# Performance work log

Measured on AMD Instinct MI355X. Metric: run time of the kernel, lower is better.

## Reference

```python
import jax, jax.numpy as jnp
import numpy as np

HEADS = 8


def setup_inputs() -> dict:
    key = jax.random.key(0)
    k0, k1, k2, k3 = jax.random.split(key, 4)
    b, c, h, w = 8, 128, 32, 32
    x = jax.random.normal(k0, (b, c, h, w), dtype=jnp.float32)
    # torch nn.Linear weights: (out_features, in_features)
    s = c ** -0.5
    wq = jax.random.normal(k1, (c, c), dtype=jnp.float32) * s
    wk = jax.random.normal(k2, (c, c), dtype=jnp.float32) * s
    wv = jax.random.normal(k3, (c, c), dtype=jnp.float32) * s
    return {"x": x, "wq": wq, "wk": wk, "wv": wv}


def reference(x, wq, wk, wv):
    b, c, h, w = x.shape
    n = HEADS
    d = c // n
    scale = d ** -0.5
    xp = jnp.transpose(x, (0, 2, 3, 1))  # (b, h, w, c)
    # torch Linear: y = x @ W.T
    q = (xp @ wq.T).reshape(b, h, w, n, d)
    k = (xp @ wk.T).reshape(b, h, w, n, d)
    v = (xp @ wv.T).reshape(b, h, w, n, d)
    # full 2D spatial attention scores: (b, n, h, w, x, y)
    weights = jnp.einsum('bhwnd,bxynd->bnhwxy', q, k) * scale
    # NOTE: original softmaxes over the LAST spatial axis (y) only
    weights = jax.nn.softmax(weights, axis=-1)
    attn = jnp.einsum('bnhwxy,bxynd->bhwnd', weights, v)
    out = attn.reshape(b, h, w, c)
    return jnp.transpose(out, (0, 3, 1, 2))  # (b, c, h, w)
```

## Files before the change

kernel.cpp:

```cpp
#include <hip/hip_runtime.h>
#include <stdint.h>


typedef __bf16 bf16x8 __attribute__((ext_vector_type(8)));
typedef float f32x16 __attribute__((ext_vector_type(16)));

#define QOFF  0u
#define KOFF  (1u << 20)
#define VOFF  (2u << 20)

static __device__ __forceinline__ unsigned short f2bf(float f) {
  union { float f; uint32_t u; } v; v.f = f;
  uint32_t r = (v.u + 0x7FFFu + ((v.u >> 16) & 1u)) >> 16;
  return (unsigned short)r;
}
static __device__ __forceinline__ uint32_t pkrne(float lo, float hi) {
  return (uint32_t)f2bf(lo) | ((uint32_t)f2bf(hi) << 16);
}
static __device__ __forceinline__ uint32_t pktrunc(float lo, float hi) {
  return (__builtin_bit_cast(uint32_t, hi) & 0xffff0000u) |
         (__builtin_bit_cast(uint32_t, lo) >> 16);
}
static __device__ __forceinline__ float fexp2(float x) {
  float r;
  asm("v_exp_f32 %0, %1" : "=v"(r) : "v"(x));
  return r;
}
static __device__ __forceinline__ f32x16 zero16() {
  f32x16 z;
#pragma unroll
  for (int i = 0; i < 16; ++i) z[i] = 0.f;
  return z;
}
static __device__ __forceinline__ int perm23(int p) {
  return (p & ~12) | ((p & 4) << 1) | ((p & 8) >> 1);
}
static __device__ __forceinline__ bf16x8 pack8(float f0, float f1, float f2,
                                               float f3, float f4, float f5,
                                               float f6, float f7) {
  uint4 u = make_uint4(pkrne(f0, f1), pkrne(f2, f3), pkrne(f4, f5), pkrne(f6, f7));
  return __builtin_bit_cast(bf16x8, u);
}

__global__ __launch_bounds__(256) void proj_kernel(
    const float* __restrict__ x, const float* __restrict__ wq,
    const float* __restrict__ wk, const float* __restrict__ wv,
    unsigned short* __restrict__ ws) {
  int bid = blockIdx.x;
  int ptile = bid & 15;
  int mat = (bid >> 4) % 3;
  int b = bid / 48;
  int t = threadIdx.x;
  int wave = t >> 6, lane = t & 63;
  int h = lane >> 5, c = lane & 31;
  int out0 = wave * 32;

  const float* w = (mat == 0) ? wq : ((mat == 1) ? wk : wv);
  const float* wrow = w + (size_t)(out0 + c) * 128 + h * 8;
  const float* xcol = x + (size_t)b * 131072 + ptile * 64 + c;

  f32x16 acc0 = zero16(), acc1 = zero16();
#pragma unroll
  for (int kt = 0; kt < 8; ++kt) {
    int ch0 = kt * 16 + h * 8;
    float4 wa = *(const float4*)(wrow + kt * 16);
    float4 wb4 = *(const float4*)(wrow + kt * 16 + 4);
    float xb0[8], xb1[8];
#pragma unroll
    for (int j = 0; j < 8; ++j) {
      xb0[j] = xcol[(size_t)(ch0 + j) * 1024];
      xb1[j] = xcol[(size_t)(ch0 + j) * 1024 + 32];
    }
    bf16x8 af = pack8(wa.x, wa.y, wa.z, wa.w, wb4.x, wb4.y, wb4.z, wb4.w);
    bf16x8 b0 = pack8(xb0[0], xb0[1], xb0[2], xb0[3], xb0[4], xb0[5], xb0[6], xb0[7]);
    bf16x8 b1 = pack8(xb1[0], xb1[1], xb1[2], xb1[3], xb1[4], xb1[5], xb1[6], xb1[7]);
    acc0 = __builtin_amdgcn_mfma_f32_32x32x16_bf16(af, b0, acc0, 0, 0, 0);
    acc1 = __builtin_amdgcn_mfma_f32_32x32x16_bf16(af, b1, acc1, 0, 0, 0);
  }

  if (mat < 2) {
    float s = (mat == 0) ? 0.36067376022224085f : 1.0f;
    unsigned short* dst = ws + ((mat == 0) ? QOFF : KOFF);
#pragma unroll
    for (int nt = 0; nt < 2; ++nt) {
      f32x16 a = nt ? acc1 : acc0;
      int p = ptile * 64 + nt * 32 + c;
#pragma unroll
      for (int rg = 0; rg < 4; ++rg) {
        int bn = b * 8 + wave * 2 + (rg >> 1);
        int dbase = ((rg & 1) ? 8 : 0) + 4 * h;
        uint32_t lo = pkrne(a[rg * 4 + 0] * s, a[rg * 4 + 1] * s);
        uint32_t hi = pkrne(a[rg * 4 + 2] * s, a[rg * 4 + 3] * s);
        *(uint2*)(dst + (size_t)bn * 16384 + (size_t)p * 16 + dbase) =
            make_uint2(lo, hi);
      }
    }
  } else {
#pragma unroll
    for (int nt = 0; nt < 2; ++nt) {
      f32x16 a = nt ? acc1 : acc0;
      int p = ptile * 64 + nt * 32 + c;
      int pp = perm23(p);
#pragma unroll
      for (int r = 0; r < 16; ++r) {
        int moff = (r & 3) + 8 * (r >> 2) + 4 * h;
        int head = (out0 + moff) >> 4;
        int d = moff & 15;
        ws[VOFF + (size_t)(b * 8 + head) * 16384 + (size_t)d * 1024 + pp] =
            f2bf(a[r]);
      }
    }
  }
}

__global__ __launch_bounds__(256) void attn_kernel(
    const unsigned short* __restrict__ ws, float* __restrict__ out) {
  int bid = blockIdx.x;
  int qc = bid & 7, bn = bid >> 3;
  const unsigned short* Qg = ws + QOFF + (size_t)bn * 16384;
  const unsigned short* Kg = ws + KOFF + (size_t)bn * 16384;
  const unsigned short* Vg = ws + VOFF + (size_t)bn * 16384;

  int t = threadIdx.x;
  int wave = t >> 6, lane = t & 63;
  int h = lane >> 5, c = lane & 31;
  int q0 = qc * 128 + wave * 32;

  bf16x8 qb = __builtin_bit_cast(
      bf16x8, *(const uint4*)(Qg + (size_t)(q0 + c) * 16 + h * 8));

  const unsigned short* kbase = Kg + (size_t)c * 16 + h * 8;
  const unsigned short* vbase = Vg + (size_t)(c & 15) * 1024 + h * 8;

  f32x16 pacc = zero16();

  bf16x8 va0_p = __builtin_bit_cast(bf16x8, *(const uint4*)(vbase));
  bf16x8 va1_p = __builtin_bit_cast(bf16x8, *(const uint4*)(vbase + 16));
  uint4 v0_c = *(const uint4*)(vbase + 32);
  uint4 v1_c = *(const uint4*)(vbase + 48);
  uint4 v0_n = *(const uint4*)(vbase + 64);
  uint4 v1_n = *(const uint4*)(vbase + 80);

  uint4 kf0 = *(const uint4*)(kbase);
  f32x16 sv0 = __builtin_amdgcn_mfma_f32_32x32x16_bf16(
      __builtin_bit_cast(bf16x8, kf0), qb, zero16(), 0, 0, 0);
  uint4 kf1 = *(const uint4*)(kbase + 512);
  f32x16 sv_cur = __builtin_amdgcn_mfma_f32_32x32x16_bf16(
      __builtin_bit_cast(bf16x8, kf1), qb, zero16(), 0, 0, 0);

  bf16x8 pm_lo, pm_hi;
  {
    float e[16];
#pragma unroll
    for (int r = 0; r < 16; ++r) e[r] = fexp2(sv0[r]);
    float s0 = (e[0] + e[1]) + (e[2] + e[3]);
    float s1 = (e[4] + e[5]) + (e[6] + e[7]);
    float s2 = (e[8] + e[9]) + (e[10] + e[11]);
    float s3 = (e[12] + e[13]) + (e[14] + e[15]);
    float sum = (s0 + s1) + (s2 + s3);
    sum += __shfl_xor(sum, 32);
    float rs = __builtin_amdgcn_rcpf(sum);
    uint32_t pm[8];
#pragma unroll
    for (int j = 0; j < 8; ++j)
      pm[j] = pktrunc(e[2 * j] * rs, e[2 * j + 1] * rs);
    pm_lo = __builtin_bit_cast(bf16x8, make_uint4(pm[0], pm[1], pm[2], pm[3]));
    pm_hi = __builtin_bit_cast(bf16x8, make_uint4(pm[4], pm[5], pm[6], pm[7]));
  }

  uint4 kf_a = *(const uint4*)(kbase + 2 * 512);
  uint4 kf_b = *(const uint4*)(kbase + 3 * 512);

#pragma unroll 2
  for (int x = 1; x < 32; ++x) {
    f32x16 sv_next = __builtin_amdgcn_mfma_f32_32x32x16_bf16(
        __builtin_bit_cast(bf16x8, kf_a), qb, zero16(), 0, 0, 0);
    kf_a = kf_b;
    int x3 = (x > 28) ? 31 : (x + 3);
    kf_b = *(const uint4*)(kbase + (size_t)x3 * 512);

    pacc = __builtin_amdgcn_mfma_f32_32x32x16_bf16(va0_p, pm_lo, pacc, 0, 0, 0);
    pacc = __builtin_amdgcn_mfma_f32_32x32x16_bf16(va1_p, pm_hi, pacc, 0, 0, 0);

    {
      float e[16];
#pragma unroll
      for (int r = 0; r < 16; ++r) e[r] = fexp2(sv_cur[r]);
      float t0 = (e[0] + e[1]) + (e[2] + e[3]);
      float t1 = (e[4] + e[5]) + (e[6] + e[7]);
      float t2 = (e[8] + e[9]) + (e[10] + e[11]);
      float t3 = (e[12] + e[13]) + (e[14] + e[15]);
      float su = (t0 + t1) + (t2 + t3);
      su += __shfl_xor(su, 32);
      float rs = __builtin_amdgcn_rcpf(su);
      uint32_t pm[8];
#pragma unroll
      for (int j = 0; j < 8; ++j)
        pm[j] = pktrunc(e[2 * j] * rs, e[2 * j + 1] * rs);
      pm_lo = __builtin_bit_cast(bf16x8, make_uint4(pm[0], pm[1], pm[2], pm[3]));
      pm_hi = __builtin_bit_cast(bf16x8, make_uint4(pm[4], pm[5], pm[6], pm[7]));
    }

    va0_p = __builtin_bit_cast(bf16x8, v0_c);
    va1_p = __builtin_bit_cast(bf16x8, v1_c);
    v0_c = v0_n; v1_c = v1_n;
    int x2 = (x > 29) ? 31 : (x + 2);
    v0_n = *(const uint4*)(vbase + x2 * 32);
    v1_n = *(const uint4*)(vbase + x2 * 32 + 16);

    sv_cur = sv_next;
  }

  pacc = __builtin_amdgcn_mfma_f32_32x32x16_bf16(va0_p, pm_lo, pacc, 0, 0, 0);
  pacc = __builtin_amdgcn_mfma_f32_32x32x16_bf16(va1_p, pm_hi, pacc, 0, 0, 0);

#pragma unroll
  for (int r = 0; r < 8; ++r) {
    int d = (r & 3) + 8 * (r >> 2) + 4 * h;
    out[(size_t)(bn * 16 + d) * 1024 + q0 + c] = pacc[r];
  }
}

extern "C" void kernel_launch(void* const* d_in, const int* in_sizes, int n_in,
                              void* d_out, int out_size, void* d_ws, size_t ws_size,
                              hipStream_t stream) {
  const float* x  = (const float*)d_in[0];
  const float* wq = (const float*)d_in[1];
  const float* wk = (const float*)d_in[2];
  const float* wv = (const float*)d_in[3];
  unsigned short* ws = (unsigned short*)d_ws;
  float* out = (float*)d_out;

  proj_kernel<<<dim3(384), dim3(256), 0, stream>>>(x, wq, wk, wv, ws);
  attn_kernel<<<dim3(512), dim3(256), 0, stream>>>(ws, out);
}
```

Before: 88.82 us.

## Compute softmax row sums via MFMA using ones rows appended to V

V is padded from 16 to 32 rows per head, and the extra rows are filled with bf16 ones. The PV matrix multiply therefore also produces the softmax denominator for each key row. This removes the per-step exp-sum reduction tree and the cross-lane shuffle, and the probabilities are no longer normalized before the bf16 cast. In exchange, the V workspace doubles, each step needs two fresh MFMAs plus VALU adds, a reciprocal and FMAs instead of a chained accumulate, and the projection kernel does extra stores.

```diff
diff --git a/kernel.cpp b/kernel.cpp
--- a/kernel.cpp
+++ b/kernel.cpp
@@ -106,9 +106,21 @@
         int moff = (r & 3) + 8 * (r >> 2) + 4 * h;
         int head = (out0 + moff) >> 4;
         int d = moff & 15;
-        ws[VOFF + (size_t)(b * 8 + head) * 16384 + (size_t)d * 1024 + pp] =
+        ws[VOFF + (size_t)(b * 8 + head) * 32768 + (size_t)d * 1024 + pp] =
             f2bf(a[r]);
       }
+    }
+    {
+      int hd = t >> 5;
+      int rr = (t & 31) >> 1;
+      int hf = t & 1;
+      unsigned short* vdst = ws + VOFF + (size_t)(b * 8 + hd) * 32768 +
+                             (size_t)(16 + rr) * 1024 + ptile * 64 + hf * 32;
+      uint4 ones = make_uint4(0x3F803F80u, 0x3F803F80u, 0x3F803F80u, 0x3F803F80u);
+      *(uint4*)(vdst) = ones;
+      *(uint4*)(vdst + 8) = ones;
+      *(uint4*)(vdst + 16) = ones;
+      *(uint4*)(vdst + 24) = ones;
     }
   }
 }
@@ -119,7 +131,7 @@
   int qc = bid & 7, bn = bid >> 3;
   const unsigned short* Qg = ws + QOFF + (size_t)bn * 16384;
   const unsigned short* Kg = ws + KOFF + (size_t)bn * 16384;
-  const unsigned short* Vg = ws + VOFF + (size_t)bn * 16384;
+  const unsigned short* Vg = ws + VOFF + (size_t)bn * 32768;
 
   int t = threadIdx.x;
   int wave = t >> 6, lane = t & 63;
@@ -130,9 +142,11 @@
       bf16x8, *(const uint4*)(Qg + (size_t)(q0 + c) * 16 + h * 8));
 
   const unsigned short* kbase = Kg + (size_t)c * 16 + h * 8;
-  const unsigned short* vbase = Vg + (size_t)(c & 15) * 1024 + h * 8;
-
-  f32x16 pacc = zero16();
+  const unsigned short* vbase = Vg + (size_t)c * 1024 + h * 8;
+
+  float acc[8];
+#pragma unroll
+  for (int r = 0; r < 8; ++r) acc[r] = 0.f;
 
   bf16x8 va0_p = __builtin_bit_cast(bf16x8, *(const uint4*)(vbase));
   bf16x8 va1_p = __builtin_bit_cast(bf16x8, *(const uint4*)(vbase + 16));
@@ -150,20 +164,10 @@
 
   bf16x8 pm_lo, pm_hi;
   {
-    float e[16];
-#pragma unroll
-    for (int r = 0; r < 16; ++r) e[r] = fexp2(sv0[r]);
-    float s0 = (e[0] + e[1]) + (e[2] + e[3]);
-    float s1 = (e[4] + e[5]) + (e[6] + e[7]);
-    float s2 = (e[8] + e[9]) + (e[10] + e[11]);
-    float s3 = (e[12] + e[13]) + (e[14] + e[15]);
-    float sum = (s0 + s1) + (s2 + s3);
-    sum += __shfl_xor(sum, 32);
-    float rs = __builtin_amdgcn_rcpf(sum);
     uint32_t pm[8];
 #pragma unroll
     for (int j = 0; j < 8; ++j)
-      pm[j] = pktrunc(e[2 * j] * rs, e[2 * j + 1] * rs);
+      pm[j] = pktrunc(fexp2(sv0[2 * j]), fexp2(sv0[2 * j + 1]));
     pm_lo = __builtin_bit_cast(bf16x8, make_uint4(pm[0], pm[1], pm[2], pm[3]));
     pm_hi = __builtin_bit_cast(bf16x8, make_uint4(pm[4], pm[5], pm[6], pm[7]));
   }
@@ -179,26 +183,22 @@
     int x3 = (x > 28) ? 31 : (x + 3);
     kf_b = *(const uint4*)(kbase + (size_t)x3 * 512);
 
-    pacc = __builtin_amdgcn_mfma_f32_32x32x16_bf16(va0_p, pm_lo, pacc, 0, 0, 0);
-    pacc = __builtin_amdgcn_mfma_f32_32x32x16_bf16(va1_p, pm_hi, pacc, 0, 0, 0);
+    f32x16 pv0 = __builtin_amdgcn_mfma_f32_32x32x16_bf16(va0_p, pm_lo, zero16(), 0, 0, 0);
+    f32x16 pv1 = __builtin_amdgcn_mfma_f32_32x32x16_bf16(va1_p, pm_hi, zero16(), 0, 0, 0);
 
     {
-      float e[16];
-#pragma unroll
-      for (int r = 0; r < 16; ++r) e[r] = fexp2(sv_cur[r]);
-      float t0 = (e[0] + e[1]) + (e[2] + e[3]);
-      float t1 = (e[4] + e[5]) + (e[6] + e[7]);
-      float t2 = (e[8] + e[9]) + (e[10] + e[11]);
-      float t3 = (e[12] + e[13]) + (e[14] + e[15]);
-      float su = (t0 + t1) + (t2 + t3);
-      su += __shfl_xor(su, 32);
-      float rs = __builtin_amdgcn_rcpf(su);
       uint32_t pm[8];
 #pragma unroll
       for (int j = 0; j < 8; ++j)
-        pm[j] = pktrunc(e[2 * j] * rs, e[2 * j + 1] * rs);
+        pm[j] = pktrunc(fexp2(sv_cur[2 * j]), fexp2(sv_cur[2 * j + 1]));
       pm_lo = __builtin_bit_cast(bf16x8, make_uint4(pm[0], pm[1], pm[2], pm[3]));
       pm_hi = __builtin_bit_cast(bf16x8, make_uint4(pm[4], pm[5], pm[6], pm[7]));
+    }
+
+    {
+      float rs = __builtin_amdgcn_rcpf(pv0[8] + pv1[8]);
+#pragma unroll
+      for (int r = 0; r < 8; ++r) acc[r] = fmaf(rs, pv0[r] + pv1[r], acc[r]);
     }
 
     va0_p = __builtin_bit_cast(bf16x8, v0_c);
@@ -211,13 +211,18 @@
     sv_cur = sv_next;
   }
 
-  pacc = __builtin_amdgcn_mfma_f32_32x32x16_bf16(va0_p, pm_lo, pacc, 0, 0, 0);
-  pacc = __builtin_amdgcn_mfma_f32_32x32x16_bf16(va1_p, pm_hi, pacc, 0, 0, 0);
+  {
+    f32x16 pv0 = __builtin_amdgcn_mfma_f32_32x32x16_bf16(va0_p, pm_lo, zero16(), 0, 0, 0);
+    f32x16 pv1 = __builtin_amdgcn_mfma_f32_32x32x16_bf16(va1_p, pm_hi, zero16(), 0, 0, 0);
+    float rs = __builtin_amdgcn_rcpf(pv0[8] + pv1[8]);
+#pragma unroll
+    for (int r = 0; r < 8; ++r) acc[r] = fmaf(rs, pv0[r] + pv1[r], acc[r]);
+  }
 
 #pragma unroll
   for (int r = 0; r < 8; ++r) {
     int d = (r & 3) + 8 * (r >> 2) + 4 * h;
-    out[(size_t)(bn * 16 + d) * 1024 + q0 + c] = pacc[r];
+    out[(size_t)(bn * 16 + d) * 1024 + q0 + c] = acc[r];
   }
 }
 
```

Result: no change. 89.35 us (+0.6%).

## Stage x tile in shared memory as bf16 and halve projection tile width

Applied to the files above, without the earlier changes.

The projection kernel now loads a 128-channel by 32-pixel tile of x with coalesced float4 reads, converts it to bf16 in LDS, and builds the MFMA B operands from LDS instead of strided scalar global loads. The pixel tile shrinks from 64 to 32 so the grid doubles to 768 blocks with one accumulator per wave. This targets uncoalesced global loads and low block count, at the cost of re-reading weights twice as often and adding a barrier plus LDS reads with possible bank conflicts.

```diff
diff --git a/kernel.cpp b/kernel.cpp
--- a/kernel.cpp
+++ b/kernel.cpp
@@ -47,68 +47,70 @@
     const float* __restrict__ wk, const float* __restrict__ wv,
     unsigned short* __restrict__ ws) {
   int bid = blockIdx.x;
-  int ptile = bid & 15;
-  int mat = (bid >> 4) % 3;
-  int b = bid / 48;
+  int pt = bid & 31;
+  int mat = (bid >> 5) % 3;
+  int b = bid / 96;
   int t = threadIdx.x;
   int wave = t >> 6, lane = t & 63;
   int h = lane >> 5, c = lane & 31;
   int out0 = wave * 32;
+  int p0 = pt * 32;
+
+  __shared__ unsigned short xs[128][32];
+
+  {
+    const float* xb = x + (size_t)b * 131072 + p0;
+#pragma unroll
+    for (int it = 0; it < 4; ++it) {
+      int ch = (t >> 3) + 32 * it;
+      int pc = (t & 7) * 4;
+      float4 v = *(const float4*)(xb + (size_t)ch * 1024 + pc);
+      *(uint2*)(&xs[ch][pc]) = make_uint2(pkrne(v.x, v.y), pkrne(v.z, v.w));
+    }
+  }
+  __syncthreads();
 
   const float* w = (mat == 0) ? wq : ((mat == 1) ? wk : wv);
   const float* wrow = w + (size_t)(out0 + c) * 128 + h * 8;
-  const float* xcol = x + (size_t)b * 131072 + ptile * 64 + c;
-
-  f32x16 acc0 = zero16(), acc1 = zero16();
+
+  f32x16 acc = zero16();
 #pragma unroll
   for (int kt = 0; kt < 8; ++kt) {
     int ch0 = kt * 16 + h * 8;
     float4 wa = *(const float4*)(wrow + kt * 16);
     float4 wb4 = *(const float4*)(wrow + kt * 16 + 4);
-    float xb0[8], xb1[8];
-#pragma unroll
-    for (int j = 0; j < 8; ++j) {
-      xb0[j] = xcol[(size_t)(ch0 + j) * 1024];
-      xb1[j] = xcol[(size_t)(ch0 + j) * 1024 + 32];
-    }
     bf16x8 af = pack8(wa.x, wa.y, wa.z, wa.w, wb4.x, wb4.y, wb4.z, wb4.w);
-    bf16x8 b0 = pack8(xb0[0], xb0[1], xb0[2], xb0[3], xb0[4], xb0[5], xb0[6], xb0[7]);
-    bf16x8 b1 = pack8(xb1[0], xb1[1], xb1[2], xb1[3], xb1[4], xb1[5], xb1[6], xb1[7]);
-    acc0 = __builtin_amdgcn_mfma_f32_32x32x16_bf16(af, b0, acc0, 0, 0, 0);
-    acc1 = __builtin_amdgcn_mfma_f32_32x32x16_bf16(af, b1, acc1, 0, 0, 0);
-  }
-
+    uint4 u;
+    u.x = (uint32_t)xs[ch0 + 0][c] | ((uint32_t)xs[ch0 + 1][c] << 16);
+    u.y = (uint32_t)xs[ch0 + 2][c] | ((uint32_t)xs[ch0 + 3][c] << 16);
+    u.z = (uint32_t)xs[ch0 + 4][c] | ((uint32_t)xs[ch0 + 5][c] << 16);
+    u.w = (uint32_t)xs[ch0 + 6][c] | ((uint32_t)xs[ch0 + 7][c] << 16);
+    bf16x8 bf = __builtin_bit_cast(bf16x8, u);
+    acc = __builtin_amdgcn_mfma_f32_32x32x16_bf16(af, bf, acc, 0, 0, 0);
+  }
+
+  int p = p0 + c;
   if (mat < 2) {
     float s = (mat == 0) ? 0.36067376022224085f : 1.0f;
     unsigned short* dst = ws + ((mat == 0) ? QOFF : KOFF);
 #pragma unroll
-    for (int nt = 0; nt < 2; ++nt) {
-      f32x16 a = nt ? acc1 : acc0;
-      int p = ptile * 64 + nt * 32 + c;
-#pragma unroll
-      for (int rg = 0; rg < 4; ++rg) {
-        int bn = b * 8 + wave * 2 + (rg >> 1);
-        int dbase = ((rg & 1) ? 8 : 0) + 4 * h;
-        uint32_t lo = pkrne(a[rg * 4 + 0] * s, a[rg * 4 + 1] * s);
-        uint32_t hi = pkrne(a[rg * 4 + 2] * s, a[rg * 4 + 3] * s);
-        *(uint2*)(dst + (size_t)bn * 16384 + (size_t)p * 16 + dbase) =
-            make_uint2(lo, hi);
-      }
+    for (int rg = 0; rg < 4; ++rg) {
+      int bn = b * 8 + wave * 2 + (rg >> 1);
+      int dbase = ((rg & 1) ? 8 : 0) + 4 * h;
+      uint32_t lo = pkrne(acc[rg * 4 + 0] * s, acc[rg * 4 + 1] * s);
+      uint32_t hi = pkrne(acc[rg * 4 + 2] * s, acc[rg * 4 + 3] * s);
+      *(uint2*)(dst + (size_t)bn * 16384 + (size_t)p * 16 + dbase) =
+          make_uint2(lo, hi);
     }
   } else {
-#pragma unroll
-    for (int nt = 0; nt < 2; ++nt) {
-      f32x16 a = nt ? acc1 : acc0;
-      int p = ptile * 64 + nt * 32 + c;
-      int pp = perm23(p);
-#pragma unroll
-      for (int r = 0; r < 16; ++r) {
-        int moff = (r & 3) + 8 * (r >> 2) + 4 * h;
-        int head = (out0 + moff) >> 4;
-        int d = moff & 15;
-        ws[VOFF + (size_t)(b * 8 + head) * 16384 + (size_t)d * 1024 + pp] =
-            f2bf(a[r]);
-      }
+    int pp = perm23(p);
+#pragma unroll
+    for (int r = 0; r < 16; ++r) {
+      int moff = (r & 3) + 8 * (r >> 2) + 4 * h;
+      int head = (out0 + moff) >> 4;
+      int d = moff & 15;
+      ws[VOFF + (size_t)(b * 8 + head) * 16384 + (size_t)d * 1024 + pp] =
+          f2bf(acc[r]);
     }
   }
 }
@@ -231,6 +233,6 @@
   unsigned short* ws = (unsigned short*)d_ws;
   float* out = (float*)d_out;
 
-  proj_kernel<<<dim3(384), dim3(256), 0, stream>>>(x, wq, wk, wv, ws);
+  proj_kernel<<<dim3(768), dim3(256), 0, stream>>>(x, wq, wk, wv, ws);
   attn_kernel<<<dim3(512), dim3(256), 0, stream>>>(ws, out);
 }
```

After: 90.00 us. No clear change (+1.3%).
